# Optimization experiments

Measured on AMD Instinct MI355X. Metric: run time of the kernel, lower is better.

The kernel has to match this reference:

```python
import jax, jax.numpy as jnp
import numpy as np

V = 32000   # vocab
E = 512     # hidden_size (d_model)
NH = 8      # num_heads
DH = E // NH
NL = 2      # num_layers
FF = 2048   # TransformerDecoderLayer default dim_feedforward
MAXLEN = 24 # cfg.max_length -> gen_len (no target given)
S, B = 48, 8
TRANS = 14
INIT = TRANS - 2            # tgt = transform[1:-1]
LF = INIT + MAXLEN - 1      # final tgt length after the loop
EPS = 1e-5
NEG = -1e9


def pos_encoding(length, d):
    pos = np.arange(length, dtype=np.float32)[:, None]
    div = np.exp(-np.log(10000.0) * np.arange(0, d, 2, dtype=np.float32) / d)
    pe = np.zeros((length, d), dtype=np.float32)
    pe[:, 0::2] = np.sin(pos * div)
    pe[:, 1::2] = np.cos(pos * div)
    return jnp.asarray(pe)


def setup_inputs() -> dict:
    key = jax.random.key(0)
    ks = jax.random.split(key, 12)
    s = 0.02
    return {
        "enc_outputs": jax.random.normal(ks[0], (S, B, E), jnp.float32),
        "transform": jax.random.randint(ks[1], (TRANS, B), 0, V),
        "tf_ratio": 0,
        "emb_table": jax.random.normal(ks[2], (V, E), jnp.float32) * s,
        "sa_w": jax.random.normal(ks[3], (NL, 3 * E, E), jnp.float32) * s,
        "sa_b": jnp.zeros((NL, 3 * E), jnp.float32),
        "sa_ow": jax.random.normal(ks[4], (NL, E, E), jnp.float32) * s,
        "sa_ob": jnp.zeros((NL, E), jnp.float32),
        "ca_w": jax.random.normal(ks[5], (NL, 3 * E, E), jnp.float32) * s,
        "ca_b": jnp.zeros((NL, 3 * E), jnp.float32),
        "ca_ow": jax.random.normal(ks[6], (NL, E, E), jnp.float32) * s,
        "ca_ob": jnp.zeros((NL, E), jnp.float32),
        "ff1_w": jax.random.normal(ks[7], (NL, FF, E), jnp.float32) * s,
        "ff1_b": jnp.zeros((NL, FF), jnp.float32),
        "ff2_w": jax.random.normal(ks[8], (NL, E, FF), jnp.float32) * s,
        "ff2_b": jnp.zeros((NL, E), jnp.float32),
        "ln_g": jnp.ones((NL, 3, E), jnp.float32),
        "ln_b": jnp.zeros((NL, 3, E), jnp.float32),
        "out_w": jax.random.normal(ks[9], (V, E), jnp.float32) * s,
        "out_b": jnp.zeros((V,), jnp.float32),
    }


def _ln(x, g, b):
    m = jnp.mean(x, -1, keepdims=True)
    v = jnp.mean((x - m) ** 2, -1, keepdims=True)
    return (x - m) * jax.lax.rsqrt(v + EPS) * g + b


def _mha(q_in, kv_in, w, b, ow, ob, mask):
    # q_in [Lq,B,E], kv_in [Lk,B,E]; PyTorch packed in_proj [3E,E]
    wq, wk, wv = jnp.split(w, 3, 0)
    bq, bk, bv = jnp.split(b, 3, 0)
    proj = lambda x, wm, bm: (x @ wm.T + bm).reshape(x.shape[0], x.shape[1], NH, DH)
    q, k, v = proj(q_in, wq, bq), proj(kv_in, wk, bk), proj(kv_in, wv, bv)
    sc = jnp.einsum('qbhd,kbhd->bhqk', q, k) / np.sqrt(DH).astype(np.float32)
    if mask is not None:
        sc = sc + mask
    a = jax.nn.softmax(sc, -1)
    o = jnp.einsum('bhqk,kbhd->qbhd', a, v).reshape(q_in.shape[0], q_in.shape[1], E)
    return o @ ow.T + ob


def _decoder(x, mem, mask, p):
    # post-norm TransformerDecoderLayer: self-attn -> cross-attn -> relu FFN
    for l in range(NL):
        x = _ln(x + _mha(x, x, p['sa_w'][l], p['sa_b'][l], p['sa_ow'][l], p['sa_ob'][l], mask),
                p['ln_g'][l, 0], p['ln_b'][l, 0])
        x = _ln(x + _mha(x, mem, p['ca_w'][l], p['ca_b'][l], p['ca_ow'][l], p['ca_ob'][l], None),
                p['ln_g'][l, 1], p['ln_b'][l, 1])
        h = jax.nn.relu(x @ p['ff1_w'][l].T + p['ff1_b'][l]) @ p['ff2_w'][l].T + p['ff2_b'][l]
        x = _ln(x + h, p['ln_g'][l, 2], p['ln_b'][l, 2])
    return x


def reference(enc_outputs, transform, tf_ratio, emb_table, sa_w, sa_b, sa_ow, sa_ob,
              ca_w, ca_b, ca_ow, ca_ob, ff1_w, ff1_b, ff2_w, ff2_b, ln_g, ln_b,
              out_w, out_b):
    # tf_ratio == 0 -> no teacher forcing; gen_len = max_length (no target attr)
    p = dict(sa_w=sa_w, sa_b=sa_b, sa_ow=sa_ow, sa_ob=sa_ob, ca_w=ca_w, ca_b=ca_b,
             ca_ow=ca_ow, ca_ob=ca_ob, ff1_w=ff1_w, ff1_b=ff1_b, ff2_w=ff2_w,
             ff2_b=ff2_b, ln_g=ln_g, ln_b=ln_b)
    pe = pos_encoding(MAXLEN, E)
    # causal mask over the fixed-size buffer; padded (future) slots cannot
    # influence valid positions, so full-buffer passes == torch prefix passes.
    mask = jnp.where(jnp.tril(jnp.ones((LF, LF), bool)), 0.0, NEG)
    tgt0 = emb_table[transform[1:-1]] + pe[:INIT][:, None, :]   # [INIT,B,E]
    buf = jnp.zeros((LF, B, E), jnp.float32).at[:INIT].set(tgt0)

    def step(buf, i):
        h = _decoder(buf, enc_outputs, mask, p)
        pos = INIT - 1 + i                        # last valid position
        pred = jnp.argmax(h[pos] @ out_w.T + out_b, axis=-1)   # [B]
        # torch re-embeds the single predicted token -> PE position 0
        emb = emb_table[pred] + pe[0]
        return buf.at[pos + 1].set(emb), None

    buf, _ = jax.lax.scan(step, buf, jnp.arange(MAXLEN - 1))
    h = _decoder(buf, enc_outputs, mask, p)       # final loop iteration's pass
    return h @ out_w.T + out_b                    # dec_outputs [LF,B,V]
```

## Files before the change

### kernel.cpp

```cpp
#include <hip/hip_runtime.h>
#include <hip/hip_bf16.h>
#include <math.h>

#define V    32000
#define E    512
#define NH   8
#define DH   64
#define NL   2
#define FF   2048
#define MAXLEN 24
#define S    48
#define B    8
#define TRANS 14
#define INIT 12
#define LF   35

#define NB   256
#define NT   1024

typedef float f4 __attribute__((ext_vector_type(4)));

__device__ inline float wsum(float v) {
#pragma unroll
  for (int off = 32; off; off >>= 1) v += __shfl_xor(v, off);
  return v;
}
__device__ inline float wmax(float v) {
#pragma unroll
  for (int off = 32; off; off >>= 1) v = fmaxf(v, __shfl_xor(v, off));
  return v;
}

__device__ inline void stc(float* p, float v) {
  __hip_atomic_store(p, v, __ATOMIC_RELAXED, __HIP_MEMORY_SCOPE_AGENT);
}
__device__ inline void stc8(float* p, float x, float y) {
  union { unsigned long long u; float f[2]; } c; c.f[0] = x; c.f[1] = y;
  __hip_atomic_store((unsigned long long*)p, c.u, __ATOMIC_RELAXED, __HIP_MEMORY_SCOPE_AGENT);
}
__device__ inline int ldci(const int* p) {
  return __hip_atomic_load(p, __ATOMIC_RELAXED, __HIP_MEMORY_SCOPE_AGENT);
}
__device__ inline void stci(int* p, int v) {
  __hip_atomic_store(p, v, __ATOMIC_RELAXED, __HIP_MEMORY_SCOPE_AGENT);
}

#define CMB(v, idx, ov, oi) do { if ((ov) > (v) || ((ov) == (v) && (oi) < (idx))) { (v) = (ov); (idx) = (oi); } } while (0)

__global__ void embed_init_k(const int* __restrict__ transform, const float* __restrict__ emb,
                             float* __restrict__ xbuf) {
  int t = blockIdx.x;
  int pos = t >> 3, b = t & 7;
  int tok = transform[(1 + pos) * B + b];
  for (int d = threadIdx.x; d < E; d += blockDim.x) {
    double div = exp(-log(10000.0) * (double)(d & ~1) / (double)E);
    double ang = (double)pos * div;
    float pe = (d & 1) ? (float)cos(ang) : (float)sin(ang);
    xbuf[(size_t)t * E + d] = emb[(size_t)tok * E + d] + pe;
  }
}

#define B_QKV 0
#define B_OW  6144
#define B_CQ  8192
#define B_COW 10240
#define B_FF1 12288
#define B_FF2 20480
#define SW_TOT 28672
#define SLOTS_PER_STEP 23
#define NSTAGE 41

#define PRE_L   688128
#define PQ_OFF  0
#define PATTS   49152
#define PRAWS   98304
#define PX1     147456
#define PQC     196608
#define PATTC   245760
#define PRAWC   294912
#define PX2     344064
#define PY      393216
#define PX3     442368
#define PHB     491520

__global__ __launch_bounds__(NT, 1) void decode_persist_k(
    const float* __restrict__ enc, const float* __restrict__ emb,
    const float* __restrict__ sa_w, const float* __restrict__ sa_b,
    const float* __restrict__ sa_ow, const float* __restrict__ sa_ob,
    const float* __restrict__ ca_w, const float* __restrict__ ca_b,
    const float* __restrict__ ca_ow, const float* __restrict__ ca_ob,
    const float* __restrict__ ff1_w, const float* __restrict__ ff1_b,
    const float* __restrict__ ff2_w, const float* __restrict__ ff2_b,
    const float* __restrict__ ln_g, const float* __restrict__ ln_b,
    const float* __restrict__ out_w, const float* __restrict__ out_b,
    const float* __restrict__ xpre, float* __restrict__ pre, float* __restrict__ amax_pre,
    float* __restrict__ kself, float* __restrict__ vself,
    float* __restrict__ kcross, float* __restrict__ vcross,
    float* __restrict__ arena, float* __restrict__ outp, int* __restrict__ bar) {
  __shared__ __align__(16) float s_w[SW_TOT];
  __shared__ __align__(16) float s_x[8 * E];
  __shared__ __align__(16) float s_raw[8 * E];
  __shared__ __align__(16) float s_q2[64];
  __shared__ __align__(16) float s_attw[64];
  __shared__ __align__(16) float s_part[4][64];
  __shared__ int   s_tok[8];
  __shared__ float s_pv[16][8];
  __shared__ int   s_pi[16][8];

  const int tid  = threadIdx.x;
  const int lane = tid & 63;
  const int wv   = tid >> 6;
  const int bid  = blockIdx.x;
  const size_t CROSS_SZ = (size_t)S * B * E;

  auto slot = [&](int st, int s) -> float* {
    return arena + ((size_t)st * SLOTS_PER_STEP + s) * 4096;
  };
  auto flg = [&](int s, int j) -> int* { return &bar[(s * 256 + j) * 16]; };
  auto set_flag = [&](int s, int tgt, bool producer) {
    __syncthreads();
    if (producer && tid == 0) stci(flg(s, bid), tgt);
  };
  auto wait_flags = [&](int s, int base, int count, int tgt) {
    if (wv == 0) {
      const int m = count - 1;
      for (;;) {
        bool ok = true;
        for (int f = lane; f < count; f += 64)
          ok &= (ldci(flg(s, base + ((f + bid) & m))) >= tgt);
        if (__all(ok)) break;
        __builtin_amdgcn_s_sleep(12);
      }
    }
    __syncthreads();
  };
  auto stage_raw = [&](const float* src) {
    const float4* s4 = (const float4*)src;
    float4* d4 = (float4*)s_raw;
    for (int k = tid; k < 1024; k += NT) d4[k] = s4[k];
    __syncthreads();
  };
  auto ln_vec = [&](const float* xa, const float* xb, int lnidx, float* dst) {
    const float* gg = ln_g + (size_t)lnidx * E;
    const float* be = ln_b + (size_t)lnidx * E;
    float v[8]; float sum = 0.f;
#pragma unroll
    for (int j = 0; j < 8; ++j) {
      int d = lane + 64 * j;
      v[j] = xa[d] + xb[d];
      sum += v[j];
    }
    sum = wsum(sum);
    float mean = sum * (1.f / 512.f);
    float d2 = 0.f;
#pragma unroll
    for (int j = 0; j < 8; ++j) { float dd = v[j] - mean; d2 += dd * dd; }
    d2 = wsum(d2);
    float inv = 1.f / sqrtf(d2 * (1.f / 512.f) + 1e-5f);
#pragma unroll
    for (int j = 0; j < 8; ++j) {
      int d = lane + 64 * j;
      stc(&dst[d], (v[j] - mean) * inv * gg[d] + be[d]);
    }
  };
  auto pproj = [&](const float* Wb, const float* biasp, const float* src, float* dst) {
    int j = wv >> 3, tt = wv & 7;
    int r = bid * 2 + j;
    const f4* wp = (const f4*)(Wb + (size_t)r * E);
    f4 w0 = wp[lane], w1 = wp[lane + 64];
    float bias = biasp[r];
    for (int g = 0; g < 12; ++g) {
      stage_raw(src + (size_t)g * 8 * E);
      const f4* x4 = (const f4*)&s_raw[tt * E];
      f4 a = w0 * x4[lane] + w1 * x4[lane + 64];
      float acc = a.x + a.y + a.z + a.w;
      acc = wsum(acc);
      if (lane == 0) stc(&dst[(size_t)(g * 8 + tt) * E + r], acc + bias);
      __syncthreads();
    }
  };

  {
    for (int l = 0; l < NL; ++l) {
      const int rr = (bid >> 2) * 16 + wv;
      const int sec = rr >> 9, off = rr & 511;
      const f4* wp = (const f4*)(ca_w + ((size_t)l * 1536 + 512 + rr) * E);
      f4 w0 = wp[lane], w1 = wp[lane + 64];
      float bias = ca_b[(size_t)l * 1536 + 512 + rr];
      float* dst = (sec == 0 ? kcross : vcross) + (size_t)l * CROSS_SZ;
      for (int g = 0; g < 12; ++g) {
        int t0 = (bid & 3) * 96 + g * 8;
        stage_raw(enc + (size_t)t0 * E);
        for (int tt = 0; tt < 8; ++tt) {
          const f4* x4 = (const f4*)&s_raw[tt * E];
          f4 a = w0 * x4[lane] + w1 * x4[lane + 64];
          float acc = a.x + a.y + a.z + a.w;
          acc = wsum(acc);
          if (lane == 0) stc(&dst[(size_t)(t0 + tt) * E + off], acc + bias);
        }
        __syncthreads();
      }
    }
    set_flag(39, 1, true);

    for (int l = 0; l < NL; ++l) {
      const int PB = 17 + l * 11;
      float* PL = pre + (size_t)l * PRE_L;
      float* q_l = PL + PQ_OFF;  float* attS_l = PL + PATTS; float* rawS_l = PL + PRAWS;
      float* x1_l = PL + PX1;    float* qc_l = PL + PQC;     float* attC_l = PL + PATTC;
      float* rawC_l = PL + PRAWC; float* x2_l = PL + PX2;    float* y_l = PL + PY;
      float* x3_l = PL + PX3;    float* hb_l = PL + PHB;
      const float* xsrc = (l == 0) ? xpre : (pre + PX3);

      if (l == 1) wait_flags(17 + 10, 0, 128, 1);
      {
        int j = wv >> 1, bg = (wv & 1) * 4;
        int r = bid * 6 + j, sec = r >> 9, off = r & 511;
        f4 w0, w1; float bias = 0.f;
        if (wv < 12) {
          const f4* wp = (const f4*)(sa_w + ((size_t)l * 1536 + r) * E);
          w0 = wp[lane]; w1 = wp[lane + 64];
          bias = sa_b[(size_t)l * 1536 + r];
        }
        for (int g = 0; g < 12; ++g) {
          stage_raw(xsrc + (size_t)g * 8 * E);
          if (wv < 12) {
            for (int tt = bg; tt < bg + 4; ++tt) {
              const f4* x4 = (const f4*)&s_raw[tt * E];
              f4 a = w0 * x4[lane] + w1 * x4[lane + 64];
              float acc = a.x + a.y + a.z + a.w;
              acc = wsum(acc);
              if (lane == 0) {
                int t = g * 8 + tt; acc += bias;
                if (sec == 0) stc(&q_l[(size_t)t * E + off], acc);
                else if (sec == 1) stc(&kself[((size_t)l * LF * B + t) * E + off], acc);
                else stc(&vself[((size_t)l * LF * B + t) * E + off], acc);
              }
            }
          }
          __syncthreads();
        }
      }
      set_flag(PB + 0, 1, true);
      wait_flags(PB + 0, 0, 256, 1);
      if (bid < 48) {
        int u = bid * 16 + wv, qi = u >> 6, rr = u & 63, b = rr >> 3, h = rr & 7;
        int nk = qi + 1;
        float qv = q_l[(size_t)(qi * 8 + b) * E + h * DH + lane];
        float sc = -INFINITY;
        for (int k = 0; k < nk; ++k) {
          float pr = wsum(qv * kself[((size_t)l * LF * B + k * 8 + b) * E + h * DH + lane]);
          if (lane == k) sc = pr * 0.125f;
        }
        float m = wmax(sc);
        float e = (lane < nk) ? expf(sc - m) : 0.f;
        float den = wsum(e);
        float aa = e / den, o = 0.f;
        for (int k = 0; k < nk; ++k) {
          float ak = __shfl(aa, k);
          o = fmaf(ak, vself[((size_t)l * LF * B + k * 8 + b) * E + h * DH + lane], o);
        }
        stc(&attS_l[(size_t)(qi * 8 + b) * E + h * DH + lane], o);
      }
      set_flag(PB + 1, 1, bid < 64);
      wait_flags(PB + 1, 0, 64, 1);
      pproj(sa_ow + (size_t)l * 512 * E, sa_ob + (size_t)l * 512, attS_l, rawS_l);
      set_flag(PB + 2, 1, true);
      wait_flags(PB + 2, 0, 256, 1);
      if (bid < 96 && wv == 0)
        ln_vec(xsrc + (size_t)bid * E, rawS_l + (size_t)bid * E, l * 3 + 0, x1_l + (size_t)bid * E);
      set_flag(PB + 3, 1, bid < 128);
      wait_flags(PB + 3, 0, 128, 1);
      pproj(ca_w + (size_t)l * 1536 * E, ca_b + (size_t)l * 1536, x1_l, qc_l);
      set_flag(PB + 4, 1, true);
      wait_flags(PB + 4, 0, 256, 1);
      wait_flags(39, 0, 256, 1);
      if (bid < 48) {
        int u = bid * 16 + wv, qi = u >> 6, rr = u & 63, b = rr >> 3, h = rr & 7;
        const float* Kc = kcross + (size_t)l * CROSS_SZ;
        const float* Vc = vcross + (size_t)l * CROSS_SZ;
        float qv = qc_l[(size_t)(qi * 8 + b) * E + h * DH + lane];
        float sc = -INFINITY;
        for (int k = 0; k < S; ++k) {
          float pr = wsum(qv * Kc[(size_t)(k * 8 + b) * E + h * DH + lane]);
          if (lane == k) sc = pr * 0.125f;
        }
        float m = wmax(sc);
        float e = (lane < S) ? expf(sc - m) : 0.f;
        float den = wsum(e);
        float aa = e / den, o = 0.f;
        for (int k = 0; k < S; ++k) {
          float ak = __shfl(aa, k);
          o = fmaf(ak, Vc[(size_t)(k * 8 + b) * E + h * DH + lane], o);
        }
        stc(&attC_l[(size_t)(qi * 8 + b) * E + h * DH + lane], o);
      }
      set_flag(PB + 5, 1, bid < 64);
      wait_flags(PB + 5, 0, 64, 1);
      pproj(ca_ow + (size_t)l * 512 * E, ca_ob + (size_t)l * 512, attC_l, rawC_l);
      set_flag(PB + 6, 1, true);
      wait_flags(PB + 6, 0, 256, 1);
      if (bid < 96 && wv == 0)
        ln_vec(x1_l + (size_t)bid * E, rawC_l + (size_t)bid * E, l * 3 + 1, x2_l + (size_t)bid * E);
      set_flag(PB + 7, 1, bid < 128);
      wait_flags(PB + 7, 0, 128, 1);
      {
        int j = wv >> 1, bg = (wv & 1) * 4;
        int r = bid * 8 + j;
        const f4* wp = (const f4*)(ff1_w + ((size_t)l * FF + r) * E);
        f4 w0 = wp[lane], w1 = wp[lane + 64];
        float bias = ff1_b[(size_t)l * FF + r];
        for (int g = 0; g < 12; ++g) {
          stage_raw(x2_l + (size_t)g * 8 * E);
          for (int tt = bg; tt < bg + 4; ++tt) {
            const f4* x4 = (const f4*)&s_raw[tt * E];
            f4 a = w0 * x4[lane] + w1 * x4[lane + 64];
            float acc = a.x + a.y + a.z + a.w;
            acc = wsum(acc);
            if (lane == 0)
              stc(&hb_l[(size_t)(g * 8 + tt) * FF + r], fmaxf(acc + bias, 0.f));
          }
          __syncthreads();
        }
      }
      set_flag(PB + 8, 1, true);
      wait_flags(PB + 8, 0, 256, 1);
      if ((bid >> 7) == l) {
        int r0 = (bid & 127) * 4;
        for (int u = wv; u < 384; u += 16) {
          int t = u >> 2, rl = u & 3;
          const f4* h4 = (const f4*)(hb_l + (size_t)t * FF);
          const f4* wp = (const f4*)(ff2_w + ((size_t)l * 512 + r0 + rl) * FF);
          float acc = 0.f;
#pragma unroll
          for (int j = 0; j < 8; ++j) {
            f4 hv = h4[j * 64 + lane];
            f4 w = wp[j * 64 + lane];
            acc += w.x * hv.x + w.y * hv.y + w.z * hv.z + w.w * hv.w;
          }
          acc = wsum(acc);
          if (lane == 0)
            stc(&y_l[(size_t)t * E + r0 + rl], acc + ff2_b[(size_t)l * 512 + r0 + rl]);
        }
      }
      set_flag(PB + 9, 1, (bid >> 7) == l);
      wait_flags(PB + 9, l * 128, 128, 1);
      if (bid < 96 && wv == 0)
        ln_vec(x2_l + (size_t)bid * E, y_l + (size_t)bid * E, l * 3 + 2, x3_l + (size_t)bid * E);
      set_flag(PB + 10, 1, bid < 128);
    }

    wait_flags(17 + 11 + 10, 0, 128, 1);
    {
      float* s_acc = s_w;
      const float* x3f = pre + PRE_L + PX3;
      const int grp = lane >> 3, sub = lane & 7;
      const int idx = wv * 8 + grp;
      const bool valid = idx < 125;
      const int r = bid * 125 + idx;
      for (int k = tid; k < 128 * 96; k += NT) s_acc[k] = 0.f;
      __syncthreads();
      for (int half = 0; half < 2; ++half) {
        f4 w8[8];
        if (valid) {
          const f4* wrow = (const f4*)(out_w + (size_t)r * E);
#pragma unroll
          for (int j = 0; j < 8; ++j) w8[j] = wrow[(half * 8 + j) * 8 + sub];
        }
        for (int g = 0; g < 12; ++g) {
          stage_raw(x3f + (size_t)g * 8 * E);
          if (valid) {
            for (int b = 0; b < 8; ++b) {
              const f4* x4 = (const f4*)&s_raw[b * E];
              float a = 0.f;
#pragma unroll
              for (int j = 0; j < 8; ++j) {
                f4 xx = x4[(half * 8 + j) * 8 + sub];
                a += w8[j].x * xx.x + w8[j].y * xx.y + w8[j].z * xx.z + w8[j].w * xx.w;
              }
              a += __shfl_xor(a, 1);
              a += __shfl_xor(a, 2);
              a += __shfl_xor(a, 4);
              if (sub == 0) s_acc[idx * 96 + g * 8 + b] += a;
            }
          }
          __syncthreads();
        }
      }
      if (valid) {
        float bo = out_b[r];
        for (int k = sub; k < 96; k += 8)
          outp[(size_t)k * V + r] = s_acc[idx * 96 + k] + bo;
      }
      __syncthreads();
      for (int b = 0; b < 8; ++b) {
        float v = (valid && sub == 0) ? s_acc[idx * 96 + 88 + b] + out_b[r] : -INFINITY;
        int ix = (valid && sub == 0) ? r : 0x7fffffff;
#pragma unroll
        for (int off = 1; off < 64; off <<= 1) {
          float ov = __shfl_xor(v, off); int oi = __shfl_xor(ix, off);
          CMB(v, ix, ov, oi);
        }
        if (lane == 0) { s_pv[wv][b] = v; s_pi[wv][b] = ix; }
      }
      __syncthreads();
      if (wv == 0) {
        int b = lane & 7, w2 = lane >> 3;
        float v = s_pv[w2][b]; int ix = s_pi[w2][b];
        float v2 = s_pv[w2 + 8][b]; int ix2 = s_pi[w2 + 8][b];
        CMB(v, ix, v2, ix2);
#pragma unroll
        for (int off = 8; off < 64; off <<= 1) {
          float ov = __shfl_xor(v, off); int oi = __shfl_xor(ix, off);
          CMB(v, ix, ov, oi);
        }
        if (lane < 8) stc8(&amax_pre[(size_t)(bid * 8 + lane) * 2], v, (float)ix);
      }
      __syncthreads();
    }
    set_flag(40, 1, true);
  }

  {
    auto cprow = [&](const float* src, int dstf) {
      f4* d = (f4*)&s_w[dstf]; const f4* s = (const f4*)src;
      for (int k = tid; k < 128; k += NT) d[k] = s[k];
    };
    for (int l = 0; l < NL; ++l) {
      for (int j = 0; j < 6; ++j)
        cprow(sa_w + ((size_t)l * 1536 + bid * 6 + j) * E, B_QKV + (l * 6 + j) * 512);
      for (int j = 0; j < 2; ++j) {
        cprow(sa_ow + ((size_t)l * 512 + bid * 2 + j) * E, B_OW + (l * 2 + j) * 512);
        cprow(ca_w + ((size_t)l * 1536 + bid * 2 + j) * E, B_CQ + (l * 2 + j) * 512);
        cprow(ca_ow + ((size_t)l * 512 + bid * 2 + j) * E, B_COW + (l * 2 + j) * 512);
      }
      for (int j = 0; j < 8; ++j)
        cprow(ff1_w + ((size_t)l * FF + bid * 8 + j) * E, B_FF1 + (l * 8 + j) * 512);
    }
    const int lf2 = bid >> 7;
    for (int j = 0; j < 4; ++j) {
      f4* d = (f4*)&s_w[B_FF2 + j * 2048];
      const f4* s = (const f4*)(ff2_w + ((size_t)lf2 * 512 + (bid & 127) * 4 + j) * FF);
      for (int k = tid; k < 512; k += NT) d[k] = s[k];
    }
    __syncthreads();
  }

  auto lnstage = [&](int lnidx) {
    if (wv < 8) {
      const float* gg = ln_g + (size_t)lnidx * E;
      const float* be = ln_b + (size_t)lnidx * E;
      float v[8]; float sum = 0.f;
#pragma unroll
      for (int j = 0; j < 8; ++j) {
        int d = lane + 64 * j;
        v[j] = s_x[wv * E + d] + s_raw[wv * E + d];
        sum += v[j];
      }
      sum = wsum(sum);
      float mean = sum * (1.f / 512.f);
      float d2 = 0.f;
#pragma unroll
      for (int j = 0; j < 8; ++j) { float dd = v[j] - mean; d2 += dd * dd; }
      d2 = wsum(d2);
      float inv = 1.f / sqrtf(d2 * (1.f / 512.f) + 1e-5f);
#pragma unroll
      for (int j = 0; j < 8; ++j) {
        int d = lane + 64 * j;
        s_x[wv * E + d] = (v[j] - mean) * inv * gg[d] + be[d];
      }
    }
    __syncthreads();
  };
  auto proj16 = [&](int wbase, const float* srcLDS, const float* biasp, float* dst) {
    int j = wv & 1, b = wv >> 1;
    int r = bid * 2 + j;
    const f4* wp = (const f4*)&s_w[wbase + j * 512];
    f4 w0 = wp[lane], w1 = wp[lane + 64];
    const f4* x4 = (const f4*)(srcLDS + b * E);
    f4 a = w0 * x4[lane] + w1 * x4[lane + 64];
    float acc = a.x + a.y + a.z + a.w;
    acc = wsum(acc);
    if (lane == 0) stc(&dst[b * E + r], acc + biasp[r]);
  };
  auto attn_stage = [&](const float* qsrc, const float* Kbase, const float* Vbase,
                        int nk, float* attdst) {
    const int b = bid >> 3, h = bid & 7;
    if (wv == 0) {
      s_q2[lane] = qsrc[b * E + h * DH + lane];
      float sc = -INFINITY;
      if (lane < nk) {
        const f4* Kr = (const f4*)(Kbase + ((size_t)lane * B + b) * E + h * DH);
        const f4* Qp = (const f4*)s_q2;
        float a0 = 0.f;
#pragma unroll
        for (int u = 0; u < 16; ++u) {
          f4 kv = Kr[u], qq = Qp[u];
          a0 += kv.x * qq.x + kv.y * qq.y + kv.z * qq.z + kv.w * qq.w;
        }
        sc = a0 * 0.125f;
      }
      float m = wmax(sc);
      float e = (lane < nk) ? expf(sc - m) : 0.f;
      float den = wsum(e);
      s_attw[lane] = e / den;
    }
    __syncthreads();
    if (wv < 4) {
      float o = 0.f;
      for (int k = wv; k < nk; k += 4)
        o = fmaf(s_attw[k], Vbase[((size_t)k * B + b) * E + h * DH + lane], o);
      s_part[wv][lane] = o;
    }
    __syncthreads();
    if (wv == 0)
      stc(&attdst[b * E + h * DH + lane],
          s_part[0][lane] + s_part[1][lane] + s_part[2][lane] + s_part[3][lane]);
  };

  for (int i = 0; i < MAXLEN - 1; ++i) {
    const int p = INIT + i;
    const int tgt = i + 1;
    float* amax_o = slot(i, 0);

    if (i == 0) wait_flags(40, 0, 256, 1);
    else        wait_flags(16, 0, 256, i);
    {
      int bw = wv & 7;
      float v = -INFINITY; int ix = 0x7fffffff;
      const float2* ap = (i == 0) ? (const float2*)amax_pre : (const float2*)slot(i - 1, 0);
#pragma unroll
      for (int t = 0; t < 4; ++t) {
        int e = lane * 4 + t;
        float2 pr = ap[e * 8 + bw];
        CMB(v, ix, pr.x, (int)pr.y);
      }
#pragma unroll
      for (int off = 1; off < 64; off <<= 1) {
        float ov = __shfl_xor(v, off); int oi = __shfl_xor(ix, off);
        CMB(v, ix, ov, oi);
      }
      if (lane == 0 && wv < 8) s_tok[bw] = ix;
      __syncthreads();
      int b = tid >> 7, d0 = (tid & 127) * 4;
      int tok = s_tok[b];
      float4 ev = *(const float4*)(emb + (size_t)tok * E + d0);
      s_x[b * E + d0]     = ev.x;
      s_x[b * E + d0 + 1] = ev.y + 1.0f;
      s_x[b * E + d0 + 2] = ev.z;
      s_x[b * E + d0 + 3] = ev.w + 1.0f;
      __syncthreads();
    }

    for (int l = 0; l < NL; ++l) {
      const int sb = l * 8;
      float* Lb    = slot(i, 1 + l * 11);
      float* q_s   = Lb;
      float* att_s = Lb + 4096;
      float* raw_s = Lb + 8192;
      float* q_c   = Lb + 12288;
      float* att_c = Lb + 16384;
      float* raw_c = Lb + 20480;
      float* hb    = Lb + 24576;
      float* yb    = Lb + 40960;

      if (wv < 12) {
        int j = wv >> 1, bg = (wv & 1) * 4;
        int r = bid * 6 + j, sec = r >> 9, off = r & 511;
        const f4* wp = (const f4*)&s_w[B_QKV + (l * 6 + j) * 512];
        f4 w0 = wp[lane], w1 = wp[lane + 64];
        float bias = sa_b[(size_t)l * 1536 + r];
        for (int b = bg; b < bg + 4; ++b) {
          const f4* x4 = (const f4*)&s_x[b * E];
          f4 a = w0 * x4[lane] + w1 * x4[lane + 64];
          float acc = a.x + a.y + a.z + a.w;
          acc = wsum(acc);
          if (lane == 0) {
            acc += bias;
            if (sec == 0) stc(&q_s[b * E + off], acc);
            else if (sec == 1) stc(&kself[((size_t)(l * LF + p) * B + b) * E + off], acc);
            else stc(&vself[((size_t)(l * LF + p) * B + b) * E + off], acc);
          }
        }
      }
      set_flag(sb + 0, tgt, true);
      wait_flags(sb + 0, 0, 256, tgt);
      if (bid < 64)
        attn_stage(q_s, kself + (size_t)l * LF * B * E, vself + (size_t)l * LF * B * E,
                   p + 1, att_s);
      set_flag(sb + 1, tgt, bid < 64);
      wait_flags(sb + 1, 0, 64, tgt);
      stage_raw(att_s);
      proj16(B_OW + l * 1024, s_raw, sa_ob + (size_t)l * E, raw_s);
      set_flag(sb + 2, tgt, true);
      wait_flags(sb + 2, 0, 256, tgt);
      stage_raw(raw_s);
      lnstage(l * 3 + 0);
      proj16(B_CQ + l * 1024, s_x, ca_b + (size_t)l * 3 * E, q_c);
      set_flag(sb + 3, tgt, true);
      wait_flags(sb + 3, 0, 256, tgt);
      if (bid < 64)
        attn_stage(q_c, kcross + (size_t)l * CROSS_SZ, vcross + (size_t)l * CROSS_SZ,
                   S, att_c);
      set_flag(sb + 4, tgt, bid < 64);
      wait_flags(sb + 4, 0, 64, tgt);
      stage_raw(att_c);
      proj16(B_COW + l * 1024, s_raw, ca_ob + (size_t)l * E, raw_c);
      set_flag(sb + 5, tgt, true);
      wait_flags(sb + 5, 0, 256, tgt);
      stage_raw(raw_c);
      lnstage(l * 3 + 1);
      {
        int j = wv >> 1, bg = (wv & 1) * 4;
        int r = bid * 8 + j;
        const f4* wp = (const f4*)&s_w[B_FF1 + (l * 8 + j) * 512];
        f4 w0 = wp[lane], w1 = wp[lane + 64];
        float bias = ff1_b[(size_t)l * FF + r];
        for (int b = bg; b < bg + 4; ++b) {
          const f4* x4 = (const f4*)&s_x[b * E];
          f4 a = w0 * x4[lane] + w1 * x4[lane + 64];
          float acc = a.x + a.y + a.z + a.w;
          acc = wsum(acc);
          if (lane == 0) stc(&hb[b * FF + r], fmaxf(acc + bias, 0.f));
        }
      }
      set_flag(sb + 6, tgt, true);
      wait_flags(sb + 6, 0, 256, tgt);
      if ((bid >> 7) == l) {
        int b = wv >> 1, j0 = (wv & 1) * 2;
        int r0 = (bid & 127) * 4;
        const f4* h4 = (const f4*)(hb + b * FF);
        f4 hv[8];
#pragma unroll
        for (int j = 0; j < 8; ++j) hv[j] = h4[j * 64 + lane];
#pragma unroll
        for (int jr = 0; jr < 2; ++jr) {
          int rl = j0 + jr;
          const f4* wp = (const f4*)&s_w[B_FF2 + rl * 2048];
          float acc = 0.f;
#pragma unroll
          for (int j = 0; j < 8; ++j) {
            f4 w = wp[j * 64 + lane];
            acc += w.x * hv[j].x + w.y * hv[j].y + w.z * hv[j].z + w.w * hv[j].w;
          }
          acc = wsum(acc);
          if (lane == 0)
            stc(&yb[b * E + r0 + rl], acc + ff2_b[(size_t)l * 512 + r0 + rl]);
        }
      }
      set_flag(sb + 7, tgt, (bid >> 7) == l);
      wait_flags(sb + 7, l * 128, 128, tgt);
      stage_raw(yb);
      lnstage(l * 3 + 2);
    }

    {
      const int grp = lane >> 3, sub = lane & 7;
      const int idx = wv * 8 + grp;
      const bool valid = idx < 125;
      const int r = bid * 125 + idx;
      float acc[8] = {0, 0, 0, 0, 0, 0, 0, 0};
      if (valid) {
        const f4* wrow = (const f4*)(out_w + (size_t)r * E);
#pragma unroll
        for (int half = 0; half < 2; ++half) {
          f4 w8[8];
#pragma unroll
          for (int j = 0; j < 8; ++j) w8[j] = wrow[(half * 8 + j) * 8 + sub];
#pragma unroll
          for (int b = 0; b < 8; ++b) {
            const f4* x4 = (const f4*)&s_x[b * E];
            float a = 0.f;
#pragma unroll
            for (int j = 0; j < 8; ++j) {
              f4 xx = x4[(half * 8 + j) * 8 + sub];
              a += w8[j].x * xx.x + w8[j].y * xx.y + w8[j].z * xx.z + w8[j].w * xx.w;
            }
            acc[b] += a;
          }
        }
#pragma unroll
        for (int b = 0; b < 8; ++b) {
          acc[b] += __shfl_xor(acc[b], 1);
          acc[b] += __shfl_xor(acc[b], 2);
          acc[b] += __shfl_xor(acc[b], 4);
        }
        if (sub == 0) {
          float bo = out_b[r];
#pragma unroll
          for (int b = 0; b < 8; ++b) {
            acc[b] += bo;
            outp[((size_t)p * B + b) * V + r] = acc[b];
          }
        }
      }
#pragma unroll
      for (int b = 0; b < 8; ++b) {
        float v = (valid && sub == 0) ? acc[b] : -INFINITY;
        int ix = (valid && sub == 0) ? r : 0x7fffffff;
#pragma unroll
        for (int off = 1; off < 64; off <<= 1) {
          float ov = __shfl_xor(v, off); int oi = __shfl_xor(ix, off);
          CMB(v, ix, ov, oi);
        }
        if (lane == 0) { s_pv[wv][b] = v; s_pi[wv][b] = ix; }
      }
      __syncthreads();
      if (wv == 0) {
        int b = lane & 7, w2 = lane >> 3;
        float v = s_pv[w2][b]; int ix = s_pi[w2][b];
        float v2 = s_pv[w2 + 8][b]; int ix2 = s_pi[w2 + 8][b];
        CMB(v, ix, v2, ix2);
#pragma unroll
        for (int off = 8; off < 64; off <<= 1) {
          float ov = __shfl_xor(v, off); int oi = __shfl_xor(ix, off);
          CMB(v, ix, ov, oi);
        }
        if (lane < 8) stc8(&amax_o[(size_t)(bid * 8 + lane) * 2], v, (float)ix);
      }
    }
    set_flag(16, tgt, true);
  }
}

extern "C" void kernel_launch(void* const* d_in, const int* in_sizes, int n_in,
                              void* d_out, int out_size, void* d_ws, size_t ws_size,
                              hipStream_t stream) {
  const float* enc       = (const float*)d_in[0];
  const int*   transform = (const int*)d_in[1];
  const float* emb       = (const float*)d_in[3];
  const float* sa_w  = (const float*)d_in[4];
  const float* sa_b  = (const float*)d_in[5];
  const float* sa_ow = (const float*)d_in[6];
  const float* sa_ob = (const float*)d_in[7];
  const float* ca_w  = (const float*)d_in[8];
  const float* ca_b  = (const float*)d_in[9];
  const float* ca_ow = (const float*)d_in[10];
  const float* ca_ob = (const float*)d_in[11];
  const float* ff1_w = (const float*)d_in[12];
  const float* ff1_b = (const float*)d_in[13];
  const float* ff2_w = (const float*)d_in[14];
  const float* ff2_b = (const float*)d_in[15];
  const float* ln_g  = (const float*)d_in[16];
  const float* ln_b  = (const float*)d_in[17];
  const float* out_w = (const float*)d_in[18];
  const float* out_b = (const float*)d_in[19];
  float* out = (float*)d_out;

  const size_t SELF_SZ  = (size_t)LF * B * E;
  const size_t CROSS_SZ = (size_t)S * B * E;
  const size_t ARENA_SZ = (size_t)(MAXLEN - 1) * SLOTS_PER_STEP * 4096;
  const size_t FLAG_SZ  = (size_t)NSTAGE * 256 * 16;
  float* ws     = (float*)d_ws;
  float* xpre   = ws;
  float* kself  = xpre + 96 * E;
  float* vself  = kself + NL * SELF_SZ;
  float* kcross = vself + NL * SELF_SZ;
  float* vcross = kcross + NL * CROSS_SZ;
  float* arena  = vcross + NL * CROSS_SZ;
  float* pre    = arena + ARENA_SZ;
  float* amaxp  = pre + (size_t)NL * PRE_L;
  int*   bar    = (int*)(amaxp + 4096);

  hipMemsetAsync(bar, 0, FLAG_SZ * 4, stream);

  embed_init_k<<<96, 128, 0, stream>>>(transform, emb, xpre);

  decode_persist_k<<<NB, NT, 0, stream>>>(
      enc, emb, sa_w, sa_b, sa_ow, sa_ob, ca_w, ca_b, ca_ow, ca_ob,
      ff1_w, ff1_b, ff2_w, ff2_b, ln_g, ln_b, out_w, out_b,
      xpre, pre, amaxp, kself, vself, kcross, vcross, arena, out, bar);
}
```

Measured before the change: 4.664 ms.

## Read activations directly from global memory and restage vocab projection in halves

The QKV, cross-KV, output-projection and FF1 matvec loops no longer stage activation tiles into shared memory with a barrier per 8 rows. Each wave now reads its activation rows straight from global/L2 with a strided token loop, which removes twelve __syncthreads per phase. The vocab projection keeps all 16 weight vectors in registers, stages 48 rows at a time into LDS, and writes logits directly while tracking the last step's argmax candidates in registers, dropping the shared accumulator. The cost is more global/L2 traffic for activations and higher register pressure in the vocab stage.

```diff
diff --git a/kernel.cpp b/kernel.cpp
--- a/kernel.cpp
+++ b/kernel.cpp
@@ -164,19 +164,17 @@
     }
   };
   auto pproj = [&](const float* Wb, const float* biasp, const float* src, float* dst) {
-    int j = wv >> 3, tt = wv & 7;
+    int j = wv >> 3, tt0 = wv & 7;
     int r = bid * 2 + j;
     const f4* wp = (const f4*)(Wb + (size_t)r * E);
     f4 w0 = wp[lane], w1 = wp[lane + 64];
     float bias = biasp[r];
-    for (int g = 0; g < 12; ++g) {
-      stage_raw(src + (size_t)g * 8 * E);
-      const f4* x4 = (const f4*)&s_raw[tt * E];
+    for (int t = tt0; t < 96; t += 8) {
+      const f4* x4 = (const f4*)(src + (size_t)t * E);
       f4 a = w0 * x4[lane] + w1 * x4[lane + 64];
       float acc = a.x + a.y + a.z + a.w;
       acc = wsum(acc);
-      if (lane == 0) stc(&dst[(size_t)(g * 8 + tt) * E + r], acc + bias);
-      __syncthreads();
+      if (lane == 0) stc(&dst[(size_t)t * E + r], acc + bias);
     }
   };
 
@@ -188,17 +186,13 @@
       f4 w0 = wp[lane], w1 = wp[lane + 64];
       float bias = ca_b[(size_t)l * 1536 + 512 + rr];
       float* dst = (sec == 0 ? kcross : vcross) + (size_t)l * CROSS_SZ;
-      for (int g = 0; g < 12; ++g) {
-        int t0 = (bid & 3) * 96 + g * 8;
-        stage_raw(enc + (size_t)t0 * E);
-        for (int tt = 0; tt < 8; ++tt) {
-          const f4* x4 = (const f4*)&s_raw[tt * E];
-          f4 a = w0 * x4[lane] + w1 * x4[lane + 64];
-          float acc = a.x + a.y + a.z + a.w;
-          acc = wsum(acc);
-          if (lane == 0) stc(&dst[(size_t)(t0 + tt) * E + off], acc + bias);
-        }
-        __syncthreads();
+      const int t0 = (bid & 3) * 96;
+      for (int tt = 0; tt < 96; ++tt) {
+        const f4* x4 = (const f4*)(enc + (size_t)(t0 + tt) * E);
+        f4 a = w0 * x4[lane] + w1 * x4[lane + 64];
+        float acc = a.x + a.y + a.z + a.w;
+        acc = wsum(acc);
+        if (lane == 0) stc(&dst[(size_t)(t0 + tt) * E + off], acc + bias);
       }
     }
     set_flag(39, 1, true);
@@ -213,32 +207,23 @@
       const float* xsrc = (l == 0) ? xpre : (pre + PX3);
 
       if (l == 1) wait_flags(17 + 10, 0, 128, 1);
-      {
-        int j = wv >> 1, bg = (wv & 1) * 4;
+      if (wv < 12) {
+        int j = wv >> 1, parity = wv & 1;
         int r = bid * 6 + j, sec = r >> 9, off = r & 511;
-        f4 w0, w1; float bias = 0.f;
-        if (wv < 12) {
-          const f4* wp = (const f4*)(sa_w + ((size_t)l * 1536 + r) * E);
-          w0 = wp[lane]; w1 = wp[lane + 64];
-          bias = sa_b[(size_t)l * 1536 + r];
-        }
-        for (int g = 0; g < 12; ++g) {
-          stage_raw(xsrc + (size_t)g * 8 * E);
-          if (wv < 12) {
-            for (int tt = bg; tt < bg + 4; ++tt) {
-              const f4* x4 = (const f4*)&s_raw[tt * E];
-              f4 a = w0 * x4[lane] + w1 * x4[lane + 64];
-              float acc = a.x + a.y + a.z + a.w;
-              acc = wsum(acc);
-              if (lane == 0) {
-                int t = g * 8 + tt; acc += bias;
-                if (sec == 0) stc(&q_l[(size_t)t * E + off], acc);
-                else if (sec == 1) stc(&kself[((size_t)l * LF * B + t) * E + off], acc);
-                else stc(&vself[((size_t)l * LF * B + t) * E + off], acc);
-              }
-            }
+        const f4* wp = (const f4*)(sa_w + ((size_t)l * 1536 + r) * E);
+        f4 w0 = wp[lane], w1 = wp[lane + 64];
+        float bias = sa_b[(size_t)l * 1536 + r];
+        for (int t = parity; t < 96; t += 2) {
+          const f4* x4 = (const f4*)(xsrc + (size_t)t * E);
+          f4 a = w0 * x4[lane] + w1 * x4[lane + 64];
+          float acc = a.x + a.y + a.z + a.w;
+          acc = wsum(acc);
+          if (lane == 0) {
+            float v = acc + bias;
+            if (sec == 0) stc(&q_l[(size_t)t * E + off], v);
+            else if (sec == 1) stc(&kself[((size_t)l * LF * B + t) * E + off], v);
+            else stc(&vself[((size_t)l * LF * B + t) * E + off], v);
           }
-          __syncthreads();
         }
       }
       set_flag(PB + 0, 1, true);
@@ -305,22 +290,18 @@
       set_flag(PB + 7, 1, bid < 128);
       wait_flags(PB + 7, 0, 128, 1);
       {
-        int j = wv >> 1, bg = (wv & 1) * 4;
+        int j = wv >> 1, parity = wv & 1;
         int r = bid * 8 + j;
         const f4* wp = (const f4*)(ff1_w + ((size_t)l * FF + r) * E);
         f4 w0 = wp[lane], w1 = wp[lane + 64];
         float bias = ff1_b[(size_t)l * FF + r];
-        for (int g = 0; g < 12; ++g) {
-          stage_raw(x2_l + (size_t)g * 8 * E);
-          for (int tt = bg; tt < bg + 4; ++tt) {
-            const f4* x4 = (const f4*)&s_raw[tt * E];
-            f4 a = w0 * x4[lane] + w1 * x4[lane + 64];
-            float acc = a.x + a.y + a.z + a.w;
-            acc = wsum(acc);
-            if (lane == 0)
-              stc(&hb_l[(size_t)(g * 8 + tt) * FF + r], fmaxf(acc + bias, 0.f));
-          }
-          __syncthreads();
+        for (int t = parity; t < 96; t += 2) {
+          const f4* x4 = (const f4*)(x2_l + (size_t)t * E);
+          f4 a = w0 * x4[lane] + w1 * x4[lane + 64];
+          float acc = a.x + a.y + a.z + a.w;
+          acc = wsum(acc);
+          if (lane == 0)
+            stc(&hb_l[(size_t)t * FF + r], fmaxf(acc + bias, 0.f));
         }
       }
       set_flag(PB + 8, 1, true);
@@ -352,49 +333,51 @@
 
     wait_flags(17 + 11 + 10, 0, 128, 1);
     {
-      float* s_acc = s_w;
       const float* x3f = pre + PRE_L + PX3;
       const int grp = lane >> 3, sub = lane & 7;
       const int idx = wv * 8 + grp;
       const bool valid = idx < 125;
       const int r = bid * 125 + idx;
-      for (int k = tid; k < 128 * 96; k += NT) s_acc[k] = 0.f;
-      __syncthreads();
+      f4 w16[16];
+      float bo = 0.f;
+      if (valid) {
+        const f4* wrow = (const f4*)(out_w + (size_t)r * E);
+#pragma unroll
+        for (int j = 0; j < 16; ++j) w16[j] = wrow[j * 8 + sub];
+        bo = out_b[r];
+      }
+      float amx[8];
+#pragma unroll
+      for (int b = 0; b < 8; ++b) amx[b] = -INFINITY;
       for (int half = 0; half < 2; ++half) {
-        f4 w8[8];
+        __syncthreads();
+        for (int k = tid; k < 48 * 128; k += NT)
+          ((f4*)s_w)[k] = ((const f4*)(x3f + (size_t)half * 48 * E))[k];
+        __syncthreads();
         if (valid) {
-          const f4* wrow = (const f4*)(out_w + (size_t)r * E);
-#pragma unroll
-          for (int j = 0; j < 8; ++j) w8[j] = wrow[(half * 8 + j) * 8 + sub];
-        }
-        for (int g = 0; g < 12; ++g) {
-          stage_raw(x3f + (size_t)g * 8 * E);
-          if (valid) {
-            for (int b = 0; b < 8; ++b) {
-              const f4* x4 = (const f4*)&s_raw[b * E];
-              float a = 0.f;
-#pragma unroll
-              for (int j = 0; j < 8; ++j) {
-                f4 xx = x4[(half * 8 + j) * 8 + sub];
-                a += w8[j].x * xx.x + w8[j].y * xx.y + w8[j].z * xx.z + w8[j].w * xx.w;
-              }
-              a += __shfl_xor(a, 1);
-              a += __shfl_xor(a, 2);
-              a += __shfl_xor(a, 4);
-              if (sub == 0) s_acc[idx * 96 + g * 8 + b] += a;
+          for (int tt = 0; tt < 48; ++tt) {
+            const f4* x4 = (const f4*)&s_w[tt * E];
+            float a = 0.f;
+#pragma unroll
+            for (int j = 0; j < 16; ++j) {
+              f4 xx = x4[j * 8 + sub];
+              a += w16[j].x * xx.x + w16[j].y * xx.y + w16[j].z * xx.z + w16[j].w * xx.w;
+            }
+            a += __shfl_xor(a, 1);
+            a += __shfl_xor(a, 2);
+            a += __shfl_xor(a, 4);
+            if (sub == 0) {
+              int t = half * 48 + tt;
+              float val = a + bo;
+              outp[(size_t)t * V + r] = val;
+              if (t >= 88) amx[t - 88] = val;
             }
           }
-          __syncthreads();
-        }
-      }
-      if (valid) {
-        float bo = out_b[r];
-        for (int k = sub; k < 96; k += 8)
-          outp[(size_t)k * V + r] = s_acc[idx * 96 + k] + bo;
+        }
       }
       __syncthreads();
       for (int b = 0; b < 8; ++b) {
-        float v = (valid && sub == 0) ? s_acc[idx * 96 + 88 + b] + out_b[r] : -INFINITY;
+        float v = (valid && sub == 0) ? amx[b] : -INFINITY;
         int ix = (valid && sub == 0) ? r : 0x7fffffff;
 #pragma unroll
         for (int off = 1; off < 64; off <<= 1) {
```

Result: no change. 4.655 ms (-0.2%).
